# Performance work log

Measured on AMD Instinct MI355X. Metric: run time of the kernel, lower is better.

The kernel has to match this reference:

```python
import jax, jax.numpy as jnp
import numpy as np
import math

N = 50000
E = 800000
HID = 128
HEADS = 8
DK = HID // HEADS
EPS_LN = 1e-5


def setup_inputs() -> dict:
    key = jax.random.key(0)
    ks = jax.random.split(key, 20)
    s = 1.0 / math.sqrt(HID)
    inp = {
        'x': jax.random.normal(ks[0], (N, HID), jnp.float32),
        'Wq': jax.random.normal(ks[1], (HID, HID), jnp.float32) * s,
        'bq': jnp.zeros((HID,), jnp.float32),
        'Wk': jax.random.normal(ks[2], (HID, HID), jnp.float32) * s,
        'bk': jnp.zeros((HID,), jnp.float32),
        'Wv': jax.random.normal(ks[3], (HID, HID), jnp.float32) * s,
        'bv': jnp.zeros((HID,), jnp.float32),
        'Wo': jax.random.normal(ks[4], (HID, HID), jnp.float32) * s,
        'bo': jnp.zeros((HID,), jnp.float32),
        'ln1_g': jnp.ones((HID,), jnp.float32),
        'ln1_b': jnp.zeros((HID,), jnp.float32),
        'W1': jax.random.normal(ks[5], (HID, 4 * HID), jnp.float32) * s,
        'b1': jnp.zeros((4 * HID,), jnp.float32),
        'W2': jax.random.normal(ks[6], (4 * HID, HID), jnp.float32) * (0.5 * s),
        'b2': jnp.zeros((HID,), jnp.float32),
        'ln2_g': jnp.ones((HID,), jnp.float32),
        'ln2_b': jnp.zeros((HID,), jnp.float32),
        'edge_index': jax.random.randint(ks[7], (2, E), 0, N, jnp.int64 if jax.config.jax_enable_x64 else jnp.int32),
    }
    return inp


def _layer_norm(x, g, b):
    mu = jnp.mean(x, axis=-1, keepdims=True)
    var = jnp.mean(jnp.square(x - mu), axis=-1, keepdims=True)
    return (x - mu) * jax.lax.rsqrt(var + EPS_LN) * g + b


def reference(x, Wq, bq, Wk, bk, Wv, bv, Wo, bo, ln1_g, ln1_b, W1, b1, W2, b2, ln2_g, ln2_b, edge_index):
    n = x.shape[0]
    src, tgt = edge_index[0], edge_index[1]
    Q = (x @ Wq + bq).reshape(n, HEADS, DK)
    K = (x @ Wk + bk).reshape(n, HEADS, DK)
    V = (x @ Wv + bv).reshape(n, HEADS, DK)
    # per-edge scores: (E, H)
    scores = jnp.sum(Q[tgt] * K[src], axis=-1) / math.sqrt(DK)
    # segment softmax over incoming edges of each target node
    smax = jax.ops.segment_max(scores, tgt, num_segments=n)  # (N, H), -inf for empty
    sexp = jnp.exp(scores - smax[tgt])
    ssum = jax.ops.segment_sum(sexp, tgt, num_segments=n)
    alpha = sexp / (ssum[tgt] + 1e-16)  # (E, H)
    # weighted V aggregation
    messages = alpha[:, :, None] * V[src]  # (E, H, DK)
    agg = jax.ops.segment_sum(messages, tgt, num_segments=n).reshape(n, HID)
    out = agg @ Wo + bo
    h = _layer_norm(x + out, ln1_g, ln1_b)
    ff = jax.nn.relu(h @ W1 + b1) @ W2 + b2
    return _layer_norm(h + ff, ln2_g, ln2_b)
```

## Files before the change

### kernel.cpp

```cpp
#include <hip/hip_runtime.h>
#include <math.h>

typedef __attribute__((ext_vector_type(8))) short bf16x8;
typedef __attribute__((ext_vector_type(4))) float f32x4;

__device__ __forceinline__ unsigned short f2b(float f) {
    unsigned int u = __float_as_uint(f);
    unsigned int r = (u + 0x7fffu + ((u >> 16) & 1u)) >> 16;
    return (unsigned short)r;
}
__device__ __forceinline__ float blo(unsigned int w) { return __uint_as_float(w << 16); }
__device__ __forceinline__ float bhi(unsigned int w) { return __uint_as_float(w & 0xffff0000u); }
__device__ __forceinline__ float b2f(unsigned short u) { return __uint_as_float((unsigned int)u << 16); }

__device__ __forceinline__ void gload_lds16(const void* g, void* lds) {
    __builtin_amdgcn_global_load_lds(
        (const __attribute__((address_space(1))) unsigned int*)g,
        (__attribute__((address_space(3))) unsigned int*)lds, 16, 0, 0);
}

template<int K, int EPI>
__global__ __launch_bounds__(256)
void mfma_gemm(const unsigned short* __restrict__ A,
               const unsigned short* __restrict__ BT,
               const float* __restrict__ bias,
               const void* __restrict__ res,
               const float* __restrict__ lng,
               const float* __restrict__ lnb,
               void* __restrict__ outv, int M, int NC)
{
    __shared__ unsigned short As[128 * 64];
    __shared__ unsigned short Bs[128 * 64];
    const int tid  = threadIdx.x;
    const int lane = tid & 63;
    const int wid  = tid >> 6;
    const int wr = wid >> 1, wc = wid & 1;
    const int rowBase = blockIdx.x * 128;
    const int colBase = blockIdx.y * 128;

    f32x4 acc[4][4];
#pragma unroll
    for (int i = 0; i < 4; ++i)
#pragma unroll
        for (int j = 0; j < 4; ++j) acc[i][j] = (f32x4)0.f;

    int srow[4], skoff[4];
#pragma unroll
    for (int t = 0; t < 4; ++t) {
        int c = tid + t * 256;
        int r = c >> 3, cc = c & 7;
        srow[t]  = r;
        skoff[t] = ((cc ^ (r & 7)) << 3);
    }

    const int rl = lane & 15;
    const int kh = lane >> 4;

    for (int k0 = 0; k0 < K; k0 += 64) {
#pragma unroll
        for (int t = 0; t < 4; ++t) {
            int c = tid + t * 256;
            gload_lds16(A + (size_t)(rowBase + srow[t]) * K + k0 + skoff[t], &As[c * 8]);
            gload_lds16(BT + (size_t)(colBase + srow[t]) * K + k0 + skoff[t], &Bs[c * 8]);
        }
        __syncthreads();

        bf16x8 a[4][2], b[4][2];
#pragma unroll
        for (int mi = 0; mi < 4; ++mi)
#pragma unroll
            for (int kt = 0; kt < 2; ++kt) {
                a[mi][kt] = *(const bf16x8*)&As[(((wr * 64 + mi * 16 + rl) * 64) + kt * 32 + kh * 8) ^ ((rl & 7) << 3)];
                b[mi][kt] = *(const bf16x8*)&Bs[(((wc * 64 + mi * 16 + rl) * 64) + kt * 32 + kh * 8) ^ ((rl & 7) << 3)];
            }
#pragma unroll
        for (int kt = 0; kt < 2; ++kt)
#pragma unroll
            for (int mi = 0; mi < 4; ++mi)
#pragma unroll
                for (int ni = 0; ni < 4; ++ni)
                    acc[mi][ni] = __builtin_amdgcn_mfma_f32_16x16x32_bf16(a[mi][kt], b[ni][kt], acc[mi][ni], 0, 0, 0);
        __syncthreads();
    }

    if (EPI == 3 || EPI == 4) {
        float* ls = (float*)As;
        float bb[4], gg[4], be[4];
#pragma unroll
        for (int ni = 0; ni < 4; ++ni) {
            int col = wc * 64 + ni * 16 + rl;
            bb[ni] = bias[col];
            gg[ni] = lng[col];
            be[ni] = lnb[col];
        }
#pragma unroll
        for (int mi = 0; mi < 4; ++mi) {
#pragma unroll
            for (int r = 0; r < 4; ++r) {
                int lrow = wr * 64 + mi * 16 + kh * 4 + r;
                int row  = rowBase + lrow;
                float s = 0.f, ss = 0.f;
#pragma unroll
                for (int ni = 0; ni < 4; ++ni) {
                    int col = wc * 64 + ni * 16 + rl;
                    float rr = 0.f;
                    if (row < M) {
                        if (EPI == 3) rr = ((const float*)res)[(size_t)row * 128 + col];
                        else          rr = b2f(((const unsigned short*)res)[(size_t)row * 128 + col]);
                    }
                    float v = acc[mi][ni][r] + bb[ni] + rr;
                    acc[mi][ni][r] = v;
                    s += v; ss += v * v;
                }
#pragma unroll
                for (int off = 1; off < 16; off <<= 1) {
                    s  += __shfl_xor(s,  off, 64);
                    ss += __shfl_xor(ss, off, 64);
                }
                if (rl == 0) {
                    ls[lrow * 2 + wc]       = s;
                    ls[256 + lrow * 2 + wc] = ss;
                }
            }
        }
        __syncthreads();
#pragma unroll
        for (int mi = 0; mi < 4; ++mi) {
#pragma unroll
            for (int r = 0; r < 4; ++r) {
                int lrow = wr * 64 + mi * 16 + kh * 4 + r;
                int row  = rowBase + lrow;
                float s  = ls[lrow * 2] + ls[lrow * 2 + 1];
                float ss = ls[256 + lrow * 2] + ls[256 + lrow * 2 + 1];
                float mean = s * (1.f / 128.f);
                float var  = ss * (1.f / 128.f) - mean * mean;
                float rstd = rsqrtf(var + 1e-5f);
#pragma unroll
                for (int ni = 0; ni < 4; ++ni) {
                    int col = wc * 64 + ni * 16 + rl;
                    float o = (acc[mi][ni][r] - mean) * rstd * gg[ni] + be[ni];
                    if (EPI == 3) {
                        ((unsigned short*)outv)[(size_t)row * 128 + col] = (row < M) ? f2b(o) : (unsigned short)0;
                    } else {
                        if (row < M) ((float*)outv)[(size_t)row * 128 + col] = o;
                    }
                }
            }
        }
    } else {
#pragma unroll
        for (int ni = 0; ni < 4; ++ni) {
            const int col = colBase + wc * 64 + ni * 16 + rl;
            const float bv = bias[col];
#pragma unroll
            for (int mi = 0; mi < 4; ++mi) {
                const int rowb = rowBase + wr * 64 + mi * 16 + kh * 4;
#pragma unroll
                for (int r = 0; r < 4; ++r) {
                    float v = acc[mi][ni][r] + bv;
                    if (EPI == 1) v = fmaxf(v, 0.f);
                    ((unsigned short*)outv)[(size_t)(rowb + r) * NC + col] = f2b(v);
                }
            }
        }
    }
}

__global__ void cast_all(const float* __restrict__ x, unsigned short* __restrict__ xb,
                         int n, int npad, int xblocks,
                         const float* __restrict__ Wq, const float* __restrict__ Wk,
                         const float* __restrict__ Wv, const float* __restrict__ Wo,
                         const float* __restrict__ W1, const float* __restrict__ W2,
                         const float* __restrict__ bq, const float* __restrict__ bk,
                         const float* __restrict__ bv,
                         unsigned short* __restrict__ WcatT, unsigned short* __restrict__ WoT,
                         unsigned short* __restrict__ W1T, unsigned short* __restrict__ W2T,
                         float* __restrict__ bqkv)
{
    if (blockIdx.x < (unsigned)xblocks) {
        size_t i = ((size_t)blockIdx.x * 256 + threadIdx.x) * 4;
        if (i >= (size_t)npad * 128) return;
        float4 v = make_float4(0.f, 0.f, 0.f, 0.f);
        if (i < (size_t)n * 128) v = *(const float4*)(x + i);
        ushort4 o;
        o.x = f2b(v.x); o.y = f2b(v.y); o.z = f2b(v.z); o.w = f2b(v.w);
        *(ushort4*)(xb + i) = o;
        return;
    }
    int i = (blockIdx.x - xblocks) * 256 + threadIdx.x;
    if (i < 49152) {
        int j = i >> 7, k = i & 127;
        const float* W = (j < 128) ? Wq : ((j < 256) ? Wk : Wv);
        WcatT[i] = f2b(W[k * 128 + (j & 127)]);
    } else if (i < 65536) {
        int t = i - 49152; int j = t >> 7, k = t & 127;
        WoT[t] = f2b(Wo[k * 128 + j]);
    } else if (i < 131072) {
        int t = i - 65536; int j = t >> 7, k = t & 127;
        W1T[t] = f2b(W1[k * 512 + j]);
    } else if (i < 196608) {
        int t = i - 131072; int j = t >> 9, k = t & 511;
        W2T[t] = f2b(W2[k * 128 + j]);
    }
    if (i < 384) bqkv[i] = (i < 128) ? bq[i] : ((i < 256) ? bk[i - 128] : bv[i - 256]);
}

#define EPB 8192

__global__ __launch_bounds__(512)
void bucket_count(const int* __restrict__ tgt, int* __restrict__ bcnt, int E, int nb)
{
    __shared__ int hist[1024];
    int base = blockIdx.x * EPB;
    for (int i = threadIdx.x; i < nb; i += 512) hist[i] = 0;
    __syncthreads();
    int end = min(base + EPB, E);
    for (int e = base + threadIdx.x; e < end; e += 512)
        atomicAdd(&hist[tgt[e] >> 6], 1);
    __syncthreads();
    for (int i = threadIdx.x; i < nb; i += 512)
        if (hist[i] > 0) atomicAdd(&bcnt[i], hist[i]);
}

__global__ __launch_bounds__(64)
void bucket_scan(const int* __restrict__ bcnt, int* __restrict__ bstart,
                 int* __restrict__ bcur, int nb, int E)
{
    int lane = threadIdx.x;
    int carry = 0;
    for (int c = 0; c < nb; c += 64) {
        int idx = c + lane;
        int v = (idx < nb) ? bcnt[idx] : 0;
        int orig = v;
#pragma unroll
        for (int off = 1; off < 64; off <<= 1) {
            int y = __shfl_up(v, off, 64);
            if (lane >= off) v += y;
        }
        if (idx < nb) { int ex = carry + v - orig; bstart[idx] = ex; bcur[idx] = ex; }
        carry += __shfl(v, 63, 64);
    }
    if (lane == 0) bstart[nb] = E;
}

__global__ __launch_bounds__(512)
void bucket_group(const int* __restrict__ src, const int* __restrict__ tgt,
                  int* __restrict__ bcur, int2* __restrict__ stage, int E, int nb)
{
    __shared__ int2 eb[EPB];
    __shared__ int hist[1024], lofs[1024], lcur[1024], gbase[1024];
    int base = blockIdx.x * EPB;
    int tid = threadIdx.x;
    for (int i = tid; i < nb; i += 512) { hist[i] = 0; lcur[i] = 0; }
    __syncthreads();
    int end = min(base + EPB, E);
    for (int e = base + tid; e < end; e += 512)
        atomicAdd(&hist[tgt[e] >> 6], 1);
    __syncthreads();
    if (tid < 64) {
        int carry = 0;
        for (int c = 0; c < nb; c += 64) {
            int idx = c + tid;
            int v = (idx < nb) ? hist[idx] : 0;
            int orig = v;
#pragma unroll
            for (int off = 1; off < 64; off <<= 1) {
                int y = __shfl_up(v, off, 64);
                if (tid >= off) v += y;
            }
            if (idx < nb) lofs[idx] = carry + v - orig;
            carry += __shfl(v, 63, 64);
        }
    }
    __syncthreads();
    for (int e = base + tid; e < end; e += 512) {
        int t = tgt[e], b = t >> 6;
        int r = atomicAdd(&lcur[b], 1);
        eb[lofs[b] + r] = make_int2(src[e], t);
    }
    __syncthreads();
    for (int i = tid; i < nb; i += 512)
        if (hist[i] > 0) gbase[i] = atomicAdd(&bcur[i], hist[i]);
    __syncthreads();
    int cnt = end - base;
    for (int i = tid; i < cnt; i += 512) {
        int2 v = eb[i];
        int b = v.y >> 6;
        stage[gbase[b] + (i - lofs[b])] = v;
    }
}

__global__ __launch_bounds__(256)
void bucket_sort(const int2* __restrict__ stage, const int* __restrict__ bstart,
                 int* __restrict__ rowp, int2* __restrict__ epos, int n, int nb)
{
    __shared__ int2 eb[3072], eb2[3072];
    __shared__ int tcnt[64], tofs[64], tcur[64];
    int b = blockIdx.x;
    int t0 = b << 6;
    if (t0 >= n) return;
    int t1 = min(t0 + 64, n);
    int s0 = bstart[b], s1 = bstart[b + 1];
    int cnt = s1 - s0;
    int tid = threadIdx.x;
    if (tid < 64) { tcnt[tid] = 0; tcur[tid] = 0; }
    __syncthreads();
    bool fits = (cnt <= 3072);
    if (fits) {
        for (int i = tid; i < cnt; i += 256) {
            int2 v = stage[s0 + i];
            eb[i] = v;
            atomicAdd(&tcnt[v.y - t0], 1);
        }
    } else {
        for (int i = tid; i < cnt; i += 256)
            atomicAdd(&tcnt[stage[s0 + i].y - t0], 1);
    }
    __syncthreads();
    if (tid < 64) {
        int v = tcnt[tid], orig = v;
#pragma unroll
        for (int off = 1; off < 64; off <<= 1) {
            int y = __shfl_up(v, off, 64);
            if (tid >= off) v += y;
        }
        tofs[tid] = v - orig;
        int t = t0 + tid;
        if (t < t1) rowp[t] = s0 + v - orig;
        if (t == n - 1) rowp[n] = s1;
    }
    __syncthreads();
    if (fits) {
        for (int i = tid; i < cnt; i += 256) {
            int2 v = eb[i];
            int lt = v.y - t0;
            int r = atomicAdd(&tcur[lt], 1);
            eb2[tofs[lt] + r] = v;
        }
        __syncthreads();
        for (int i = tid; i < cnt; i += 256) epos[s0 + i] = eb2[i];
    } else {
        for (int i = tid; i < cnt; i += 256) {
            int2 v = stage[s0 + i];
            int lt = v.y - t0;
            int r = atomicAdd(&tcur[lt], 1);
            epos[s0 + tofs[lt] + r] = v;
        }
    }
}

#define SCORE_SCALE 0.360673760222241f

__global__ __launch_bounds__(256)
void score_kernel(const unsigned short* __restrict__ qkv, const int2* __restrict__ epos,
                  float* __restrict__ scores, int E)
{
    int gw = (blockIdx.x * 256 + threadIdx.x) >> 4;
    int el = threadIdx.x & 15;
    if (gw >= E) return;
    int2 st = epos[gw];
    uint4 qv = *(const uint4*)(qkv + (size_t)st.y * 384 + el * 8);
    uint4 kv = *(const uint4*)(qkv + (size_t)st.x * 384 + 128 + el * 8);
    float d;
    d  = blo(qv.x) * blo(kv.x) + bhi(qv.x) * bhi(kv.x);
    d += blo(qv.y) * blo(kv.y) + bhi(qv.y) * bhi(kv.y);
    d += blo(qv.z) * blo(kv.z) + bhi(qv.z) * bhi(kv.z);
    d += blo(qv.w) * blo(kv.w) + bhi(qv.w) * bhi(kv.w);
    d += __shfl_xor(d, 1, 64);
    if ((el & 1) == 0)
        scores[(size_t)gw * 8 + (el >> 1)] = d * SCORE_SCALE;
}

__global__ __launch_bounds__(256)
void attn_agg(const unsigned short* __restrict__ qkv, const int* __restrict__ rowp,
              const int2* __restrict__ epos, const float* __restrict__ scores,
              unsigned short* __restrict__ agg, int n, int npad)
{
    int wid  = (blockIdx.x * blockDim.x + threadIdx.x) >> 6;
    int lane = threadIdx.x & 63;
    if (wid >= npad) return;
    if (wid >= n) { *(unsigned int*)(agg + (size_t)wid * 128 + lane * 2) = 0u; return; }

    const int head = lane >> 3;
    int e = rowp[wid];
    const int e1 = rowp[wid + 1];

    float m = -INFINITY, l = 0.f, a0 = 0.f, a1 = 0.f;

    for (; e + 4 <= e1; e += 4) {
        int s0 = epos[e].x, s1 = epos[e + 1].x, s2 = epos[e + 2].x, s3 = epos[e + 3].x;
        float sc0 = scores[(size_t)e * 8 + head];
        float sc1 = scores[(size_t)(e + 1) * 8 + head];
        float sc2 = scores[(size_t)(e + 2) * 8 + head];
        float sc3 = scores[(size_t)(e + 3) * 8 + head];
        unsigned int v0 = *(const unsigned int*)(qkv + (size_t)s0 * 384 + 256 + lane * 2);
        unsigned int v1 = *(const unsigned int*)(qkv + (size_t)s1 * 384 + 256 + lane * 2);
        unsigned int v2 = *(const unsigned int*)(qkv + (size_t)s2 * 384 + 256 + lane * 2);
        unsigned int v3 = *(const unsigned int*)(qkv + (size_t)s3 * 384 + 256 + lane * 2);
        float mn = fmaxf(fmaxf(fmaxf(sc0, sc1), fmaxf(sc2, sc3)), m);
        float scale = exp2f(m - mn);
        float w0 = exp2f(sc0 - mn), w1 = exp2f(sc1 - mn);
        float w2 = exp2f(sc2 - mn), w3 = exp2f(sc3 - mn);
        l  = l * scale + ((w0 + w1) + (w2 + w3));
        a0 = a0 * scale + (w0 * blo(v0) + w1 * blo(v1)) + (w2 * blo(v2) + w3 * blo(v3));
        a1 = a1 * scale + (w0 * bhi(v0) + w1 * bhi(v1)) + (w2 * bhi(v2) + w3 * bhi(v3));
        m = mn;
    }
    for (; e < e1; ++e) {
        int s = epos[e].x;
        float sc = scores[(size_t)e * 8 + head];
        unsigned int vw = *(const unsigned int*)(qkv + (size_t)s * 384 + 256 + lane * 2);
        float mn = fmaxf(m, sc);
        float scale = exp2f(m - mn);
        float w = exp2f(sc - mn);
        l  = l * scale + w;
        a0 = a0 * scale + w * blo(vw);
        a1 = a1 * scale + w * bhi(vw);
        m = mn;
    }
    float inv = 1.f / (l + 1e-16f);
    unsigned int o = (unsigned int)f2b(a0 * inv) | ((unsigned int)f2b(a1 * inv) << 16);
    *(unsigned int*)(agg + (size_t)wid * 128 + lane * 2) = o;
}

extern "C" void kernel_launch(void* const* d_in, const int* in_sizes, int n_in,
                              void* d_out, int out_size, void* d_ws, size_t ws_size,
                              hipStream_t stream)
{
    const float* x    = (const float*)d_in[0];
    const float* Wq   = (const float*)d_in[1];
    const float* bq   = (const float*)d_in[2];
    const float* Wk   = (const float*)d_in[3];
    const float* bk   = (const float*)d_in[4];
    const float* Wv   = (const float*)d_in[5];
    const float* bv   = (const float*)d_in[6];
    const float* Wo   = (const float*)d_in[7];
    const float* bo   = (const float*)d_in[8];
    const float* ln1g = (const float*)d_in[9];
    const float* ln1b = (const float*)d_in[10];
    const float* W1   = (const float*)d_in[11];
    const float* b1   = (const float*)d_in[12];
    const float* W2   = (const float*)d_in[13];
    const float* b2   = (const float*)d_in[14];
    const float* ln2g = (const float*)d_in[15];
    const float* ln2b = (const float*)d_in[16];
    const int*   eidx = (const int*)d_in[17];

    const int N_ = in_sizes[0] / 128;
    const int E_ = in_sizes[17] / 2;
    const int Mpad = ((N_ + 127) / 128) * 128;
    const int nb = (N_ + 63) >> 6;
    const int* srcE = eidx;
    const int* tgtE = eidx + E_;
    float* out = (float*)d_out;

    unsigned short* xb   = (unsigned short*)d_ws;
    unsigned short* qkvb = xb + (size_t)Mpad * 128;
    unsigned short* tb   = xb;
    unsigned short* aggb = qkvb + (size_t)Mpad * 384;
    unsigned short* hb   = aggb + (size_t)Mpad * 128;
    float* scores        = (float*)(hb + (size_t)Mpad * 128);
    unsigned short* WcatT = (unsigned short*)(scores + (size_t)E_ * 8);
    unsigned short* WoT  = WcatT + 384 * 128;
    unsigned short* W1T  = WoT + 128 * 128;
    unsigned short* W2T  = W1T + 512 * 128;
    float* bqkv          = (float*)(W2T + 128 * 512);
    int2* stage          = (int2*)(bqkv + 384);
    int2* epos           = stage + E_;
    int* bcnt   = (int*)(epos + E_);
    int* bstart = bcnt + 1024;
    int* bcur   = bstart + 1025;
    int* rowp   = bcur + 1024;

    hipMemsetAsync(bcnt, 0, sizeof(int) * 1024, stream);

    const int xblocks = (int)(((size_t)Mpad * 128 / 4 + 255) / 256);
    const int gblocks = (E_ + EPB - 1) / EPB;

    cast_all<<<xblocks + 768, 256, 0, stream>>>(x, xb, N_, Mpad, xblocks,
                                                Wq, Wk, Wv, Wo, W1, W2, bq, bk, bv,
                                                WcatT, WoT, W1T, W2T, bqkv);

    mfma_gemm<128, 2><<<dim3(Mpad / 128, 3), 256, 0, stream>>>(
        xb, WcatT, bqkv, nullptr, nullptr, nullptr, qkvb, N_, 384);

    bucket_count<<<gblocks, 512, 0, stream>>>(tgtE, bcnt, E_, nb);
    bucket_scan<<<1, 64, 0, stream>>>(bcnt, bstart, bcur, nb, E_);
    bucket_group<<<gblocks, 512, 0, stream>>>(srcE, tgtE, bcur, stage, E_, nb);
    bucket_sort<<<nb, 256, 0, stream>>>(stage, bstart, rowp, epos, N_, nb);

    score_kernel<<<((size_t)E_ * 16 + 255) / 256, 256, 0, stream>>>(qkvb, epos, scores, E_);
    attn_agg<<<(Mpad + 3) / 4, 256, 0, stream>>>(qkvb, rowp, epos, scores, aggb, N_, Mpad);

    mfma_gemm<128, 3><<<dim3(Mpad / 128, 1), 256, 0, stream>>>(
        aggb, WoT, bo, x, ln1g, ln1b, hb, N_, 128);

    mfma_gemm<128, 1><<<dim3(Mpad / 128, 4), 256, 0, stream>>>(
        hb, W1T, b1, nullptr, nullptr, nullptr, tb, N_, 512);

    mfma_gemm<512, 4><<<dim3(Mpad / 128, 1), 256, 0, stream>>>(
        tb, W2T, b2, hb, ln2g, ln2b, out, N_, 128);
}
```

Measured before the change: 220.7 us.

## Double-buffer GEMM LDS tiles and move segment softmax into a separate kernel

```diff
diff --git a/kernel.cpp b/kernel.cpp
--- a/kernel.cpp
+++ b/kernel.cpp
@@ -29,8 +29,8 @@
                const float* __restrict__ lnb,
                void* __restrict__ outv, int M, int NC)
 {
-    __shared__ unsigned short As[128 * 64];
-    __shared__ unsigned short Bs[128 * 64];
+    __shared__ unsigned short As[2][128 * 64];
+    __shared__ unsigned short Bs[2][128 * 64];
     const int tid  = threadIdx.x;
     const int lane = tid & 63;
     const int wid  = tid >> 6;
@@ -55,23 +55,36 @@
 
     const int rl = lane & 15;
     const int kh = lane >> 4;
-
-    for (int k0 = 0; k0 < K; k0 += 64) {
-#pragma unroll
-        for (int t = 0; t < 4; ++t) {
-            int c = tid + t * 256;
-            gload_lds16(A + (size_t)(rowBase + srow[t]) * K + k0 + skoff[t], &As[c * 8]);
-            gload_lds16(BT + (size_t)(colBase + srow[t]) * K + k0 + skoff[t], &Bs[c * 8]);
-        }
-        __syncthreads();
-
+    constexpr int NT = K / 64;
+
+#pragma unroll
+    for (int u = 0; u < 4; ++u) {
+        int c = tid + u * 256;
+        gload_lds16(A + (size_t)(rowBase + srow[u]) * K + skoff[u], &As[0][c * 8]);
+        gload_lds16(BT + (size_t)(colBase + srow[u]) * K + skoff[u], &Bs[0][c * 8]);
+    }
+    __syncthreads();
+
+#pragma unroll
+    for (int t = 0; t < NT; ++t) {
+        if (t + 1 < NT) {
+            const int nb = (t + 1) & 1;
+            const int k0 = (t + 1) * 64;
+#pragma unroll
+            for (int u = 0; u < 4; ++u) {
+                int c = tid + u * 256;
+                gload_lds16(A + (size_t)(rowBase + srow[u]) * K + k0 + skoff[u], &As[nb][c * 8]);
+                gload_lds16(BT + (size_t)(colBase + srow[u]) * K + k0 + skoff[u], &Bs[nb][c * 8]);
+            }
+        }
+        const int cb = t & 1;
         bf16x8 a[4][2], b[4][2];
 #pragma unroll
         for (int mi = 0; mi < 4; ++mi)
 #pragma unroll
             for (int kt = 0; kt < 2; ++kt) {
-                a[mi][kt] = *(const bf16x8*)&As[(((wr * 64 + mi * 16 + rl) * 64) + kt * 32 + kh * 8) ^ ((rl & 7) << 3)];
-                b[mi][kt] = *(const bf16x8*)&Bs[(((wc * 64 + mi * 16 + rl) * 64) + kt * 32 + kh * 8) ^ ((rl & 7) << 3)];
+                a[mi][kt] = *(const bf16x8*)&As[cb][(((wr * 64 + mi * 16 + rl) * 64) + kt * 32 + kh * 8) ^ ((rl & 7) << 3)];
+                b[mi][kt] = *(const bf16x8*)&Bs[cb][(((wc * 64 + mi * 16 + rl) * 64) + kt * 32 + kh * 8) ^ ((rl & 7) << 3)];
             }
 #pragma unroll
         for (int kt = 0; kt < 2; ++kt)
@@ -84,7 +97,7 @@
     }
 
     if (EPI == 3 || EPI == 4) {
-        float* ls = (float*)As;
+        float* ls = (float*)&As[0][0];
         float bb[4], gg[4], be[4];
 #pragma unroll
         for (int ni = 0; ni < 4; ++ni) {
@@ -372,8 +385,30 @@
 }
 
 __global__ __launch_bounds__(256)
+void softmax_kernel(const int* __restrict__ rowp, float* __restrict__ sc, int n)
+{
+    int b = blockIdx.x;
+#pragma unroll
+    for (int pp = 0; pp < 2; ++pp) {
+        int p = threadIdx.x + pp * 256;
+        int lt = p >> 3, h = p & 7;
+        int t = (b << 6) + lt;
+        if (t >= n) continue;
+        int e0 = rowp[t], e1 = rowp[t + 1];
+        if (e0 >= e1) continue;
+        float m = -INFINITY;
+        for (int e = e0; e < e1; ++e) m = fmaxf(m, sc[(size_t)e * 8 + h]);
+        float s = 0.f;
+        for (int e = e0; e < e1; ++e) s += exp2f(sc[(size_t)e * 8 + h] - m);
+        float inv = 1.f / (s + 1e-16f);
+        for (int e = e0; e < e1; ++e)
+            sc[(size_t)e * 8 + h] = exp2f(sc[(size_t)e * 8 + h] - m) * inv;
+    }
+}
+
+__global__ __launch_bounds__(256)
 void attn_agg(const unsigned short* __restrict__ qkv, const int* __restrict__ rowp,
-              const int2* __restrict__ epos, const float* __restrict__ scores,
+              const int2* __restrict__ epos, const float* __restrict__ wsc,
               unsigned short* __restrict__ agg, int n, int npad)
 {
     int wid  = (blockIdx.x * blockDim.x + threadIdx.x) >> 6;
@@ -385,41 +420,29 @@
     int e = rowp[wid];
     const int e1 = rowp[wid + 1];
 
-    float m = -INFINITY, l = 0.f, a0 = 0.f, a1 = 0.f;
+    float a0 = 0.f, a1 = 0.f;
 
     for (; e + 4 <= e1; e += 4) {
         int s0 = epos[e].x, s1 = epos[e + 1].x, s2 = epos[e + 2].x, s3 = epos[e + 3].x;
-        float sc0 = scores[(size_t)e * 8 + head];
-        float sc1 = scores[(size_t)(e + 1) * 8 + head];
-        float sc2 = scores[(size_t)(e + 2) * 8 + head];
-        float sc3 = scores[(size_t)(e + 3) * 8 + head];
+        float w0 = wsc[(size_t)e * 8 + head];
+        float w1 = wsc[(size_t)(e + 1) * 8 + head];
+        float w2 = wsc[(size_t)(e + 2) * 8 + head];
+        float w3 = wsc[(size_t)(e + 3) * 8 + head];
         unsigned int v0 = *(const unsigned int*)(qkv + (size_t)s0 * 384 + 256 + lane * 2);
         unsigned int v1 = *(const unsigned int*)(qkv + (size_t)s1 * 384 + 256 + lane * 2);
         unsigned int v2 = *(const unsigned int*)(qkv + (size_t)s2 * 384 + 256 + lane * 2);
         unsigned int v3 = *(const unsigned int*)(qkv + (size_t)s3 * 384 + 256 + lane * 2);
-        float mn = fmaxf(fmaxf(fmaxf(sc0, sc1), fmaxf(sc2, sc3)), m);
-        float scale = exp2f(m - mn);
-        float w0 = exp2f(sc0 - mn), w1 = exp2f(sc1 - mn);
-        float w2 = exp2f(sc2 - mn), w3 = exp2f(sc3 - mn);
-        l  = l * scale + ((w0 + w1) + (w2 + w3));
-        a0 = a0 * scale + (w0 * blo(v0) + w1 * blo(v1)) + (w2 * blo(v2) + w3 * blo(v3));
-        a1 = a1 * scale + (w0 * bhi(v0) + w1 * bhi(v1)) + (w2 * bhi(v2) + w3 * bhi(v3));
-        m = mn;
+        a0 += (w0 * blo(v0) + w1 * blo(v1)) + (w2 * blo(v2) + w3 * blo(v3));
+        a1 += (w0 * bhi(v0) + w1 * bhi(v1)) + (w2 * bhi(v2) + w3 * bhi(v3));
     }
     for (; e < e1; ++e) {
         int s = epos[e].x;
-        float sc = scores[(size_t)e * 8 + head];
+        float w = wsc[(size_t)e * 8 + head];
         unsigned int vw = *(const unsigned int*)(qkv + (size_t)s * 384 + 256 + lane * 2);
-        float mn = fmaxf(m, sc);
-        float scale = exp2f(m - mn);
-        float w = exp2f(sc - mn);
-        l  = l * scale + w;
-        a0 = a0 * scale + w * blo(vw);
-        a1 = a1 * scale + w * bhi(vw);
-        m = mn;
-    }
-    float inv = 1.f / (l + 1e-16f);
-    unsigned int o = (unsigned int)f2b(a0 * inv) | ((unsigned int)f2b(a1 * inv) << 16);
+        a0 += w * blo(vw);
+        a1 += w * bhi(vw);
+    }
+    unsigned int o = (unsigned int)f2b(a0) | ((unsigned int)f2b(a1) << 16);
     *(unsigned int*)(agg + (size_t)wid * 128 + lane * 2) = o;
 }
 
@@ -490,6 +513,7 @@
     bucket_sort<<<nb, 256, 0, stream>>>(stage, bstart, rowp, epos, N_, nb);
 
     score_kernel<<<((size_t)E_ * 16 + 255) / 256, 256, 0, stream>>>(qkvb, epos, scores, E_);
+    softmax_kernel<<<nb, 256, 0, stream>>>(rowp, scores, N_);
     attn_agg<<<(Mpad + 3) / 4, 256, 0, stream>>>(qkvb, rowp, epos, scores, aggb, N_, Mpad);
 
     mfma_gemm<128, 3><<<dim3(Mpad / 128, 1), 256, 0, stream>>>(
```

After: 251.9 us. 1.14x slower.

## Fuse edge score computation into attention aggregation and merge bucket counting into cast kernel

Applied to the files above, without the earlier changes.

```diff
diff --git a/kernel.cpp b/kernel.cpp
--- a/kernel.cpp
+++ b/kernel.cpp
@@ -166,6 +166,8 @@
     }
 }
 
+#define EPB 8192
+
 __global__ void cast_all(const float* __restrict__ x, unsigned short* __restrict__ xb,
                          int n, int npad, int xblocks,
                          const float* __restrict__ Wq, const float* __restrict__ Wk,
@@ -175,8 +177,11 @@
                          const float* __restrict__ bv,
                          unsigned short* __restrict__ WcatT, unsigned short* __restrict__ WoT,
                          unsigned short* __restrict__ W1T, unsigned short* __restrict__ W2T,
-                         float* __restrict__ bqkv)
-{
+                         float* __restrict__ bqkv,
+                         const int* __restrict__ tgt, int* __restrict__ bhist,
+                         int E, int nb)
+{
+    __shared__ int hist[1024];
     if (blockIdx.x < (unsigned)xblocks) {
         size_t i = ((size_t)blockIdx.x * 256 + threadIdx.x) * 4;
         if (i >= (size_t)npad * 128) return;
@@ -187,60 +192,65 @@
         *(ushort4*)(xb + i) = o;
         return;
     }
-    int i = (blockIdx.x - xblocks) * 256 + threadIdx.x;
-    if (i < 49152) {
-        int j = i >> 7, k = i & 127;
-        const float* W = (j < 128) ? Wq : ((j < 256) ? Wk : Wv);
-        WcatT[i] = f2b(W[k * 128 + (j & 127)]);
-    } else if (i < 65536) {
-        int t = i - 49152; int j = t >> 7, k = t & 127;
-        WoT[t] = f2b(Wo[k * 128 + j]);
-    } else if (i < 131072) {
-        int t = i - 65536; int j = t >> 7, k = t & 127;
-        W1T[t] = f2b(W1[k * 512 + j]);
-    } else if (i < 196608) {
-        int t = i - 131072; int j = t >> 9, k = t & 511;
-        W2T[t] = f2b(W2[k * 128 + j]);
-    }
-    if (i < 384) bqkv[i] = (i < 128) ? bq[i] : ((i < 256) ? bk[i - 128] : bv[i - 256]);
-}
-
-#define EPB 8192
-
-__global__ __launch_bounds__(512)
-void bucket_count(const int* __restrict__ tgt, int* __restrict__ bcnt, int E, int nb)
-{
-    __shared__ int hist[1024];
-    int base = blockIdx.x * EPB;
-    for (int i = threadIdx.x; i < nb; i += 512) hist[i] = 0;
+    if (blockIdx.x < (unsigned)(xblocks + 768)) {
+        int i = (blockIdx.x - xblocks) * 256 + threadIdx.x;
+        if (i < 49152) {
+            int j = i >> 7, k = i & 127;
+            const float* W = (j < 128) ? Wq : ((j < 256) ? Wk : Wv);
+            WcatT[i] = f2b(W[k * 128 + (j & 127)]);
+        } else if (i < 65536) {
+            int t = i - 49152; int j = t >> 7, k = t & 127;
+            WoT[t] = f2b(Wo[k * 128 + j]);
+        } else if (i < 131072) {
+            int t = i - 65536; int j = t >> 7, k = t & 127;
+            W1T[t] = f2b(W1[k * 512 + j]);
+        } else if (i < 196608) {
+            int t = i - 131072; int j = t >> 9, k = t & 511;
+            W2T[t] = f2b(W2[k * 128 + j]);
+        }
+        if (i < 384) bqkv[i] = (i < 128) ? bq[i] : ((i < 256) ? bk[i - 128] : bv[i - 256]);
+        return;
+    }
+    int cb = blockIdx.x - xblocks - 768;
+    int base = cb * EPB;
+    for (int i = threadIdx.x; i < nb; i += 256) hist[i] = 0;
     __syncthreads();
     int end = min(base + EPB, E);
-    for (int e = base + threadIdx.x; e < end; e += 512)
+    for (int e = base + threadIdx.x; e < end; e += 256)
         atomicAdd(&hist[tgt[e] >> 6], 1);
     __syncthreads();
-    for (int i = threadIdx.x; i < nb; i += 512)
-        if (hist[i] > 0) atomicAdd(&bcnt[i], hist[i]);
-}
-
-__global__ __launch_bounds__(64)
-void bucket_scan(const int* __restrict__ bcnt, int* __restrict__ bstart,
-                 int* __restrict__ bcur, int nb, int E)
-{
-    int lane = threadIdx.x;
-    int carry = 0;
-    for (int c = 0; c < nb; c += 64) {
-        int idx = c + lane;
-        int v = (idx < nb) ? bcnt[idx] : 0;
-        int orig = v;
-#pragma unroll
-        for (int off = 1; off < 64; off <<= 1) {
-            int y = __shfl_up(v, off, 64);
-            if (lane >= off) v += y;
-        }
-        if (idx < nb) { int ex = carry + v - orig; bstart[idx] = ex; bcur[idx] = ex; }
-        carry += __shfl(v, 63, 64);
-    }
-    if (lane == 0) bstart[nb] = E;
+    for (int i = threadIdx.x; i < nb; i += 256)
+        bhist[cb * 1024 + i] = hist[i];
+}
+
+__global__ __launch_bounds__(256)
+void bucket_scan(const int* __restrict__ bhist, int* __restrict__ bstart,
+                 int* __restrict__ bcur, int nb, int gb, int E)
+{
+    __shared__ int colsum[1024];
+    int tid = threadIdx.x;
+    for (int i = tid; i < nb; i += 256) {
+        int v = 0;
+        for (int g = 0; g < gb; ++g) v += bhist[g * 1024 + i];
+        colsum[i] = v;
+    }
+    __syncthreads();
+    if (tid < 64) {
+        int carry = 0;
+        for (int c = 0; c < nb; c += 64) {
+            int idx = c + tid;
+            int v = (idx < nb) ? colsum[idx] : 0;
+            int orig = v;
+#pragma unroll
+            for (int off = 1; off < 64; off <<= 1) {
+                int y = __shfl_up(v, off, 64);
+                if (tid >= off) v += y;
+            }
+            if (idx < nb) { int ex = carry + v - orig; bstart[idx] = ex; bcur[idx] = ex; }
+            carry += __shfl(v, 63, 64);
+        }
+        if (tid == 0) bstart[nb] = E;
+    }
 }
 
 __global__ __launch_bounds__(512)
@@ -292,7 +302,7 @@
 
 __global__ __launch_bounds__(256)
 void bucket_sort(const int2* __restrict__ stage, const int* __restrict__ bstart,
-                 int* __restrict__ rowp, int2* __restrict__ epos, int n, int nb)
+                 int* __restrict__ rowp, int* __restrict__ ssrc, int n, int nb)
 {
     __shared__ int2 eb[3072], eb2[3072];
     __shared__ int tcnt[64], tofs[64], tcur[64];
@@ -338,13 +348,13 @@
             eb2[tofs[lt] + r] = v;
         }
         __syncthreads();
-        for (int i = tid; i < cnt; i += 256) epos[s0 + i] = eb2[i];
+        for (int i = tid; i < cnt; i += 256) ssrc[s0 + i] = eb2[i].x;
     } else {
         for (int i = tid; i < cnt; i += 256) {
             int2 v = stage[s0 + i];
             int lt = v.y - t0;
             int r = atomicAdd(&tcur[lt], 1);
-            epos[s0 + tofs[lt] + r] = v;
+            ssrc[s0 + tofs[lt] + r] = v.x;
         }
     }
 }
@@ -352,75 +362,80 @@
 #define SCORE_SCALE 0.360673760222241f
 
 __global__ __launch_bounds__(256)
-void score_kernel(const unsigned short* __restrict__ qkv, const int2* __restrict__ epos,
-                  float* __restrict__ scores, int E)
-{
-    int gw = (blockIdx.x * 256 + threadIdx.x) >> 4;
-    int el = threadIdx.x & 15;
-    if (gw >= E) return;
-    int2 st = epos[gw];
-    uint4 qv = *(const uint4*)(qkv + (size_t)st.y * 384 + el * 8);
-    uint4 kv = *(const uint4*)(qkv + (size_t)st.x * 384 + 128 + el * 8);
-    float d;
-    d  = blo(qv.x) * blo(kv.x) + bhi(qv.x) * bhi(kv.x);
-    d += blo(qv.y) * blo(kv.y) + bhi(qv.y) * bhi(kv.y);
-    d += blo(qv.z) * blo(kv.z) + bhi(qv.z) * bhi(kv.z);
-    d += blo(qv.w) * blo(kv.w) + bhi(qv.w) * bhi(kv.w);
-    d += __shfl_xor(d, 1, 64);
-    if ((el & 1) == 0)
-        scores[(size_t)gw * 8 + (el >> 1)] = d * SCORE_SCALE;
-}
-
-__global__ __launch_bounds__(256)
-void attn_agg(const unsigned short* __restrict__ qkv, const int* __restrict__ rowp,
-              const int2* __restrict__ epos, const float* __restrict__ scores,
-              unsigned short* __restrict__ agg, int n, int npad)
+void attn_fused(const unsigned short* __restrict__ qkv, const int* __restrict__ rowp,
+                const int* __restrict__ ssrc, unsigned short* __restrict__ agg,
+                int n, int npad)
 {
     int wid  = (blockIdx.x * blockDim.x + threadIdx.x) >> 6;
     int lane = threadIdx.x & 63;
     if (wid >= npad) return;
-    if (wid >= n) { *(unsigned int*)(agg + (size_t)wid * 128 + lane * 2) = 0u; return; }
-
-    const int head = lane >> 3;
+    const int j4 = lane & 31;
+    if (wid >= n) {
+        if (lane >= 32)
+            *(uint2*)(agg + (size_t)wid * 128 + (size_t)(lane - 32) * 4) = make_uint2(0u, 0u);
+        return;
+    }
+
+    uint2 qw = *(const uint2*)(qkv + (size_t)wid * 384 + j4 * 4);
+    const float q0 = blo(qw.x) * SCORE_SCALE, q1 = bhi(qw.x) * SCORE_SCALE;
+    const float q2 = blo(qw.y) * SCORE_SCALE, q3 = bhi(qw.y) * SCORE_SCALE;
+
     int e = rowp[wid];
     const int e1 = rowp[wid + 1];
 
-    float m = -INFINITY, l = 0.f, a0 = 0.f, a1 = 0.f;
+    float m = -1e30f, s = 0.f, a0 = 0.f, a1 = 0.f, a2 = 0.f, a3 = 0.f;
 
     for (; e + 4 <= e1; e += 4) {
-        int s0 = epos[e].x, s1 = epos[e + 1].x, s2 = epos[e + 2].x, s3 = epos[e + 3].x;
-        float sc0 = scores[(size_t)e * 8 + head];
-        float sc1 = scores[(size_t)(e + 1) * 8 + head];
-        float sc2 = scores[(size_t)(e + 2) * 8 + head];
-        float sc3 = scores[(size_t)(e + 3) * 8 + head];
-        unsigned int v0 = *(const unsigned int*)(qkv + (size_t)s0 * 384 + 256 + lane * 2);
-        unsigned int v1 = *(const unsigned int*)(qkv + (size_t)s1 * 384 + 256 + lane * 2);
-        unsigned int v2 = *(const unsigned int*)(qkv + (size_t)s2 * 384 + 256 + lane * 2);
-        unsigned int v3 = *(const unsigned int*)(qkv + (size_t)s3 * 384 + 256 + lane * 2);
+        int s0 = ssrc[e], s1 = ssrc[e + 1], s2 = ssrc[e + 2], s3 = ssrc[e + 3];
+        uint2 k0 = *(const uint2*)(qkv + (size_t)s0 * 384 + 128 + lane * 4);
+        uint2 k1 = *(const uint2*)(qkv + (size_t)s1 * 384 + 128 + lane * 4);
+        uint2 k2 = *(const uint2*)(qkv + (size_t)s2 * 384 + 128 + lane * 4);
+        uint2 k3 = *(const uint2*)(qkv + (size_t)s3 * 384 + 128 + lane * 4);
+        float p0 = q0 * blo(k0.x) + q1 * bhi(k0.x) + q2 * blo(k0.y) + q3 * bhi(k0.y);
+        float p1 = q0 * blo(k1.x) + q1 * bhi(k1.x) + q2 * blo(k1.y) + q3 * bhi(k1.y);
+        float p2 = q0 * blo(k2.x) + q1 * bhi(k2.x) + q2 * blo(k2.y) + q3 * bhi(k2.y);
+        float p3 = q0 * blo(k3.x) + q1 * bhi(k3.x) + q2 * blo(k3.y) + q3 * bhi(k3.y);
+        p0 += __shfl_xor(p0, 1, 64); p0 += __shfl_xor(p0, 2, 64);
+        p1 += __shfl_xor(p1, 1, 64); p1 += __shfl_xor(p1, 2, 64);
+        p2 += __shfl_xor(p2, 1, 64); p2 += __shfl_xor(p2, 2, 64);
+        p3 += __shfl_xor(p3, 1, 64); p3 += __shfl_xor(p3, 2, 64);
+        float sc0 = __shfl(p0, j4, 64);
+        float sc1 = __shfl(p1, j4, 64);
+        float sc2 = __shfl(p2, j4, 64);
+        float sc3 = __shfl(p3, j4, 64);
         float mn = fmaxf(fmaxf(fmaxf(sc0, sc1), fmaxf(sc2, sc3)), m);
         float scale = exp2f(m - mn);
         float w0 = exp2f(sc0 - mn), w1 = exp2f(sc1 - mn);
         float w2 = exp2f(sc2 - mn), w3 = exp2f(sc3 - mn);
-        l  = l * scale + ((w0 + w1) + (w2 + w3));
-        a0 = a0 * scale + (w0 * blo(v0) + w1 * blo(v1)) + (w2 * blo(v2) + w3 * blo(v3));
-        a1 = a1 * scale + (w0 * bhi(v0) + w1 * bhi(v1)) + (w2 * bhi(v2) + w3 * bhi(v3));
+        s  = s * scale + ((w0 + w1) + (w2 + w3));
+        a0 = a0 * scale + (w0 * blo(k0.x) + w1 * blo(k1.x)) + (w2 * blo(k2.x) + w3 * blo(k3.x));
+        a1 = a1 * scale + (w0 * bhi(k0.x) + w1 * bhi(k1.x)) + (w2 * bhi(k2.x) + w3 * bhi(k3.x));
+        a2 = a2 * scale + (w0 * blo(k0.y) + w1 * blo(k1.y)) + (w2 * blo(k2.y) + w3 * blo(k3.y));
+        a3 = a3 * scale + (w0 * bhi(k0.y) + w1 * bhi(k1.y)) + (w2 * bhi(k2.y) + w3 * bhi(k3.y));
         m = mn;
     }
     for (; e < e1; ++e) {
-        int s = epos[e].x;
-        float sc = scores[(size_t)e * 8 + head];
-        unsigned int vw = *(const unsigned int*)(qkv + (size_t)s * 384 + 256 + lane * 2);
+        int sx = ssrc[e];
+        uint2 kv = *(const uint2*)(qkv + (size_t)sx * 384 + 128 + lane * 4);
+        float p = q0 * blo(kv.x) + q1 * bhi(kv.x) + q2 * blo(kv.y) + q3 * bhi(kv.y);
+        p += __shfl_xor(p, 1, 64); p += __shfl_xor(p, 2, 64);
+        float sc = __shfl(p, j4, 64);
         float mn = fmaxf(m, sc);
         float scale = exp2f(m - mn);
         float w = exp2f(sc - mn);
-        l  = l * scale + w;
-        a0 = a0 * scale + w * blo(vw);
-        a1 = a1 * scale + w * bhi(vw);
+        s  = s * scale + w;
+        a0 = a0 * scale + w * blo(kv.x);
+        a1 = a1 * scale + w * bhi(kv.x);
+        a2 = a2 * scale + w * blo(kv.y);
+        a3 = a3 * scale + w * bhi(kv.y);
         m = mn;
     }
-    float inv = 1.f / (l + 1e-16f);
-    unsigned int o = (unsigned int)f2b(a0 * inv) | ((unsigned int)f2b(a1 * inv) << 16);
-    *(unsigned int*)(agg + (size_t)wid * 128 + lane * 2) = o;
+    float inv = 1.f / (s + 1e-16f);
+    if (lane >= 32) {
+        unsigned int o1 = (unsigned int)f2b(a0 * inv) | ((unsigned int)f2b(a1 * inv) << 16);
+        unsigned int o2 = (unsigned int)f2b(a2 * inv) | ((unsigned int)f2b(a3 * inv) << 16);
+        *(uint2*)(agg + (size_t)wid * 128 + (size_t)(lane - 32) * 4) = make_uint2(o1, o2);
+    }
 }
 
 extern "C" void kernel_launch(void* const* d_in, const int* in_sizes, int n_in,
@@ -459,38 +474,34 @@
     unsigned short* tb   = xb;
     unsigned short* aggb = qkvb + (size_t)Mpad * 384;
     unsigned short* hb   = aggb + (size_t)Mpad * 128;
-    float* scores        = (float*)(hb + (size_t)Mpad * 128);
-    unsigned short* WcatT = (unsigned short*)(scores + (size_t)E_ * 8);
+    unsigned short* WcatT = hb + (size_t)Mpad * 128;
     unsigned short* WoT  = WcatT + 384 * 128;
     unsigned short* W1T  = WoT + 128 * 128;
     unsigned short* W2T  = W1T + 512 * 128;
     float* bqkv          = (float*)(W2T + 128 * 512);
     int2* stage          = (int2*)(bqkv + 384);
-    int2* epos           = stage + E_;
-    int* bcnt   = (int*)(epos + E_);
-    int* bstart = bcnt + 1024;
+    int* ssrc   = (int*)(stage + E_);
+    int* bstart = ssrc + E_;
     int* bcur   = bstart + 1025;
     int* rowp   = bcur + 1024;
-
-    hipMemsetAsync(bcnt, 0, sizeof(int) * 1024, stream);
+    int* bhist  = rowp + N_ + 1;
 
     const int xblocks = (int)(((size_t)Mpad * 128 / 4 + 255) / 256);
     const int gblocks = (E_ + EPB - 1) / EPB;
 
-    cast_all<<<xblocks + 768, 256, 0, stream>>>(x, xb, N_, Mpad, xblocks,
-                                                Wq, Wk, Wv, Wo, W1, W2, bq, bk, bv,
-                                                WcatT, WoT, W1T, W2T, bqkv);
+    cast_all<<<xblocks + 768 + gblocks, 256, 0, stream>>>(
+        x, xb, N_, Mpad, xblocks,
+        Wq, Wk, Wv, Wo, W1, W2, bq, bk, bv,
+        WcatT, WoT, W1T, W2T, bqkv, tgtE, bhist, E_, nb);
 
     mfma_gemm<128, 2><<<dim3(Mpad / 128, 3), 256, 0, stream>>>(
         xb, WcatT, bqkv, nullptr, nullptr, nullptr, qkvb, N_, 384);
 
-    bucket_count<<<gblocks, 512, 0, stream>>>(tgtE, bcnt, E_, nb);
-    bucket_scan<<<1, 64, 0, stream>>>(bcnt, bstart, bcur, nb, E_);
+    bucket_scan<<<1, 256, 0, stream>>>(bhist, bstart, bcur, nb, gblocks, E_);
     bucket_group<<<gblocks, 512, 0, stream>>>(srcE, tgtE, bcur, stage, E_, nb);
-    bucket_sort<<<nb, 256, 0, stream>>>(stage, bstart, rowp, epos, N_, nb);
-
-    score_kernel<<<((size_t)E_ * 16 + 255) / 256, 256, 0, stream>>>(qkvb, epos, scores, E_);
-    attn_agg<<<(Mpad + 3) / 4, 256, 0, stream>>>(qkvb, rowp, epos, scores, aggb, N_, Mpad);
+    bucket_sort<<<nb, 256, 0, stream>>>(stage, bstart, rowp, ssrc, N_, nb);
+
+    attn_fused<<<(Mpad + 3) / 4, 256, 0, stream>>>(qkvb, rowp, ssrc, aggb, N_, Mpad);
 
     mfma_gemm<128, 3><<<dim3(Mpad / 128, 1), 256, 0, stream>>>(
         aggb, WoT, bo, x, ln1g, ln1b, hb, N_, 128);
```

New measurement: 256.6 us. 16.2% more time.
